# Kernel tuning notes

Measured on AMD Instinct MI355X. Metric: run time of the kernel, lower is better.

## Reference

```python
import jax, jax.numpy as jnp
import numpy as np

NUM_FREQUENCIES = 128
NUM_TIMES = 128
SIGMA = 0.1
BATCH = 32
LENGTH = 8192


def setup_inputs() -> dict:
    key = jax.random.key(0)
    signal = jax.random.normal(key, (BATCH, LENGTH), dtype=jnp.float32)
    return {"signal": signal}


def reference(signal) -> jnp.ndarray:
    # signal: [B, L]
    B, L = signal.shape
    # Matches torch.linspace(...).long(): linspace then truncate toward zero.
    time_centers = jnp.linspace(0.0, L - 1, NUM_TIMES).astype(jnp.int32).astype(jnp.float32)  # [T]
    freq_vals = jnp.linspace(0.0, L // 2, NUM_FREQUENCIES).astype(jnp.int32).astype(jnp.float32)  # [F]
    t = jnp.arange(L, dtype=jnp.float32)  # [L]
    sigma_w = SIGMA * L
    # Gaussian windows, one per time center: [T, L]
    window = jnp.exp(-0.5 * ((t[None, :] - time_centers[:, None]) / sigma_w) ** 2)
    # Real part of exp(-2j*pi*f*l/L) modulation: [F, L]
    two_pi = jnp.float32(2.0 * np.pi)
    cos_mod = jnp.cos(two_pi * freq_vals[:, None] * t[None, :] / L)
    # Original loop stores a complex dot product into a real tensor -> real part only:
    # result[b, f, t] = sum_l signal[b,l] * window[t,l] * cos(2*pi*f*l/L)
    windowed = jnp.einsum('bl,tl->btl', signal, window)  # [B, T, L]
    result = jnp.einsum('btl,fl->bft', windowed, cos_mod)  # [B, F, T]
    return result
```

## Files before the change

kernel.cpp:

```cpp
#include <hip/hip_runtime.h>
#include <hip/hip_bf16.h>
#include <math.h>


#define L_ 8192
#define B_ 32
#define SPLITK 16
#define KW 512
#define NSTEP 16

typedef _Float16 half8 __attribute__((ext_vector_type(8)));
typedef __fp16 fp16x2 __attribute__((ext_vector_type(2)));
typedef float float4v __attribute__((ext_vector_type(4)));

#define H_ 0.001220703125f
#define CSTEP_ 7.66990393942594528198e-4f


__global__ __launch_bounds__(256, 2) void gabor_gemm_kernel(
    const float* __restrict__ signal, float* __restrict__ partial) {
  const int bx = blockIdx.x;
  const int kc = bx & 15;
  const int bgrp = (bx >> 4) & 7;
  const int th = (bx >> 7) & 1;
  const int fh = (bx >> 8) & 1;
  const int tid = threadIdx.x;
  const int lane = tid & 63;
  const int wv = tid >> 6;
  const int frow = lane & 15;
  const int quad = lane >> 4;

  __shared__ _Float16 Sg[4][KW];

  {
    const int idx = tid * 8;
    const int bi = idx >> 9;
    const int off = idx & 511;
    const float* sp = signal + (size_t)(bgrp * 4 + bi) * L_ + kc * KW + off;
    float4v s0 = *(const float4v*)sp;
    float4v s1 = *(const float4v*)(sp + 4);
    union { fp16x2 h2[4]; half8 h8; } sh;
    sh.h2[0] = __builtin_amdgcn_cvt_pkrtz(s0[0], s0[1]);
    sh.h2[1] = __builtin_amdgcn_cvt_pkrtz(s0[2], s0[3]);
    sh.h2[2] = __builtin_amdgcn_cvt_pkrtz(s1[0], s1[1]);
    sh.h2[3] = __builtin_amdgcn_cvt_pkrtz(s1[2], s1[3]);
    *(half8*)&Sg[bi][off] = sh.h8;
  }
  __syncthreads();

  const int t0 = th * 64 + (wv & 1) * 32;
  const int f0 = fh * 64 + (wv >> 1) * 32;
  const int l0 = kc * KW + quad * 8;

  float w[2][8], Rw[2][8];
  const float Q32 = __expf(-0.00152587890625f);
#pragma unroll
  for (int fr = 0; fr < 2; ++fr) {
    const float tc = truncf((float)(t0 + fr * 16 + frow) * (8191.0f / 127.0f));
#pragma unroll
    for (int j = 0; j < 8; ++j) {
      const float x = ((float)(l0 + j) - tc) * H_;
      w[fr][j] = __expf(-0.5f * x * x);
      Rw[fr][j] = __expf(__builtin_fmaf(-0.0390625f, x, -7.62939453125e-4f));
    }
  }
  float c[2][8], cp[2][8], K32[2];
#pragma unroll
  for (int fr = 0; fr < 2; ++fr) {
    const int fv = (int)((float)(f0 + fr * 16 + frow) * (4096.0f / 127.0f));
    K32[fr] = 2.0f * __cosf((float)((fv * 32) & (L_ - 1)) * CSTEP_);
#pragma unroll
    for (int j = 0; j < 8; ++j) {
      c[fr][j] = __cosf((float)((fv * (l0 + j)) & (L_ - 1)) * CSTEP_);
      cp[fr][j] = __cosf((float)((fv * (l0 + j + 8160)) & (L_ - 1)) * CSTEP_);
    }
  }

  float4v acc[2][2][4];
#pragma unroll
  for (int i = 0; i < 2; ++i)
#pragma unroll
    for (int j = 0; j < 2; ++j)
#pragma unroll
      for (int bi = 0; bi < 4; ++bi) acc[i][j][bi] = (float4v)(0.0f);

#pragma unroll
  for (int s = 0; s < NSTEP; ++s) {
    union { fp16x2 h2[4]; half8 h8; } ha[2], hc[2];
#pragma unroll
    for (int fr = 0; fr < 2; ++fr)
#pragma unroll
      for (int p = 0; p < 4; ++p) {
        ha[fr].h2[p] = __builtin_amdgcn_cvt_pkrtz(w[fr][2 * p], w[fr][2 * p + 1]);
        hc[fr].h2[p] = __builtin_amdgcn_cvt_pkrtz(c[fr][2 * p], c[fr][2 * p + 1]);
      }
    half8 sgv[4];
#pragma unroll
    for (int bi = 0; bi < 4; ++bi)
      sgv[bi] = *(const half8*)&Sg[bi][s * 32 + quad * 8];
#pragma unroll
    for (int fr2 = 0; fr2 < 2; ++fr2)
#pragma unroll
      for (int bi = 0; bi < 4; ++bi) {
        const half8 hbf = hc[fr2].h8 * sgv[bi];
        acc[0][fr2][bi] = __builtin_amdgcn_mfma_f32_16x16x32_f16(
            ha[0].h8, hbf, acc[0][fr2][bi], 0, 0, 0);
        acc[1][fr2][bi] = __builtin_amdgcn_mfma_f32_16x16x32_f16(
            ha[1].h8, hbf, acc[1][fr2][bi], 0, 0, 0);
      }
    if (s + 1 < NSTEP) {
#pragma unroll
      for (int fr = 0; fr < 2; ++fr)
#pragma unroll
        for (int j = 0; j < 8; ++j) {
          w[fr][j] *= Rw[fr][j];
          Rw[fr][j] *= Q32;
          const float cn = __builtin_fmaf(K32[fr], c[fr][j], -cp[fr][j]);
          cp[fr][j] = c[fr][j];
          c[fr][j] = cn;
        }
    }
  }

#pragma unroll
  for (int bi = 0; bi < 4; ++bi) {
    float* pbase = partial + ((size_t)(kc * B_ + bgrp * 4 + bi) << 14);
#pragma unroll
    for (int fr2 = 0; fr2 < 2; ++fr2) {
      const int f = f0 + fr2 * 16 + frow;
#pragma unroll
      for (int fr1 = 0; fr1 < 2; ++fr1) {
        const int t = t0 + fr1 * 16 + quad * 4;
        *(float4v*)(pbase + f * 128 + t) = acc[fr1][fr2][bi];
      }
    }
  }
}

__global__ __launch_bounds__(256) void gabor_reduce_kernel(
    const float* __restrict__ partial, float* __restrict__ out) {
  const size_t gi = ((size_t)blockIdx.x * 256 + threadIdx.x) * 4;
  float4v s = (float4v)(0.0f);
#pragma unroll
  for (int kc = 0; kc < SPLITK; ++kc)
    s += *(const float4v*)(partial + (size_t)kc * 524288 + gi);
  *(float4v*)(out + gi) = s;
}

extern "C" void kernel_launch(void* const* d_in, const int* in_sizes, int n_in,
                              void* d_out, int out_size, void* d_ws, size_t ws_size,
                              hipStream_t stream) {
  const float* signal = (const float*)d_in[0];
  float* out = (float*)d_out;
  float* partial = (float*)d_ws;
  gabor_gemm_kernel<<<dim3(512), dim3(256), 0, stream>>>(signal, partial);
  gabor_reduce_kernel<<<dim3(512), dim3(256), 0, stream>>>(partial, out);
}
```

Baseline: 81.17 us.

## Fuse split-K reduction into one kernel with per-batch blocks and in-block wave reduction

Replaces the two-kernel split-K scheme, which wrote 16 partial sums to global memory and then reduced them in a second kernel, with a single kernel. Each block now handles one batch row over the full length. The four waves split K, and their accumulators are summed through shared memory before a direct store to the output. The inner loop switches to packed float2 recurrences with an unroll-1 loop of 32 double steps, which cuts register pressure. In exchange, each block runs a much longer recurrence chain, which risks fp16/fp32 drift, and each wave now does one batch instead of four, so there is less reuse of the A operand per MFMA.

```diff
diff --git a/kernel.cpp b/kernel.cpp
--- a/kernel.cpp
+++ b/kernel.cpp
@@ -5,146 +5,153 @@
 
 #define L_ 8192
 #define B_ 32
-#define SPLITK 16
-#define KW 512
-#define NSTEP 16
 
 typedef _Float16 half8 __attribute__((ext_vector_type(8)));
 typedef __fp16 fp16x2 __attribute__((ext_vector_type(2)));
+typedef float float2v __attribute__((ext_vector_type(2)));
 typedef float float4v __attribute__((ext_vector_type(4)));
 
 #define H_ 0.001220703125f
 #define CSTEP_ 7.66990393942594528198e-4f
 
-
-__global__ __launch_bounds__(256, 2) void gabor_gemm_kernel(
-    const float* __restrict__ signal, float* __restrict__ partial) {
+__global__ __launch_bounds__(256, 2) void gabor_kernel(
+    const float* __restrict__ signal, float* __restrict__ out) {
   const int bx = blockIdx.x;
-  const int kc = bx & 15;
-  const int bgrp = (bx >> 4) & 7;
-  const int th = (bx >> 7) & 1;
-  const int fh = (bx >> 8) & 1;
+  const int b = bx & 31;
+  const int th = (bx >> 5) & 3;
+  const int fh = (bx >> 7) & 3;
   const int tid = threadIdx.x;
   const int lane = tid & 63;
   const int wv = tid >> 6;
   const int frow = lane & 15;
   const int quad = lane >> 4;
 
-  __shared__ _Float16 Sg[4][KW];
+  __shared__ _Float16 Sg[L_];
+  __shared__ float4v Acc[4][64][4];
 
   {
-    const int idx = tid * 8;
-    const int bi = idx >> 9;
-    const int off = idx & 511;
-    const float* sp = signal + (size_t)(bgrp * 4 + bi) * L_ + kc * KW + off;
-    float4v s0 = *(const float4v*)sp;
-    float4v s1 = *(const float4v*)(sp + 4);
-    union { fp16x2 h2[4]; half8 h8; } sh;
-    sh.h2[0] = __builtin_amdgcn_cvt_pkrtz(s0[0], s0[1]);
-    sh.h2[1] = __builtin_amdgcn_cvt_pkrtz(s0[2], s0[3]);
-    sh.h2[2] = __builtin_amdgcn_cvt_pkrtz(s1[0], s1[1]);
-    sh.h2[3] = __builtin_amdgcn_cvt_pkrtz(s1[2], s1[3]);
-    *(half8*)&Sg[bi][off] = sh.h8;
+    const float* srow = signal + (size_t)b * L_;
+#pragma unroll
+    for (int i = 0; i < 4; ++i) {
+      const int off = i * 2048 + tid * 8;
+      float4v s0 = *(const float4v*)(srow + off);
+      float4v s1 = *(const float4v*)(srow + off + 4);
+      union { fp16x2 h2[4]; half8 h8; } sh;
+      sh.h2[0] = __builtin_amdgcn_cvt_pkrtz(s0[0], s0[1]);
+      sh.h2[1] = __builtin_amdgcn_cvt_pkrtz(s0[2], s0[3]);
+      sh.h2[2] = __builtin_amdgcn_cvt_pkrtz(s1[0], s1[1]);
+      sh.h2[3] = __builtin_amdgcn_cvt_pkrtz(s1[2], s1[3]);
+      *(half8*)&Sg[off] = sh.h8;
+    }
   }
   __syncthreads();
 
-  const int t0 = th * 64 + (wv & 1) * 32;
-  const int f0 = fh * 64 + (wv >> 1) * 32;
-  const int l0 = kc * KW + quad * 8;
+  const int t0 = th * 32;
+  const int f0 = fh * 32;
+  const int k0 = wv * 2048 + quad * 8;
 
-  float w[2][8], Rw[2][8];
-  const float Q32 = __expf(-0.00152587890625f);
+  float2v w2[2][4], Rw2[2][4];
+  float2v cE2[2][4], cO2[2][4];
+  float2v K32v[2];
+  const float2v Q32v = {0.99847528338432312012f, 0.99847528338432312012f};
 #pragma unroll
   for (int fr = 0; fr < 2; ++fr) {
     const float tc = truncf((float)(t0 + fr * 16 + frow) * (8191.0f / 127.0f));
+    const int fv = (int)((float)(f0 + fr * 16 + frow) * (4096.0f / 127.0f));
+    const float K32 = 2.0f * __cosf((float)((fv * 32) & (L_ - 1)) * CSTEP_);
+    K32v[fr] = (float2v){K32, K32};
 #pragma unroll
-    for (int j = 0; j < 8; ++j) {
-      const float x = ((float)(l0 + j) - tc) * H_;
-      w[fr][j] = __expf(-0.5f * x * x);
-      Rw[fr][j] = __expf(__builtin_fmaf(-0.0390625f, x, -7.62939453125e-4f));
-    }
-  }
-  float c[2][8], cp[2][8], K32[2];
+    for (int q = 0; q < 4; ++q) {
 #pragma unroll
-  for (int fr = 0; fr < 2; ++fr) {
-    const int fv = (int)((float)(f0 + fr * 16 + frow) * (4096.0f / 127.0f));
-    K32[fr] = 2.0f * __cosf((float)((fv * 32) & (L_ - 1)) * CSTEP_);
-#pragma unroll
-    for (int j = 0; j < 8; ++j) {
-      c[fr][j] = __cosf((float)((fv * (l0 + j)) & (L_ - 1)) * CSTEP_);
-      cp[fr][j] = __cosf((float)((fv * (l0 + j + 8160)) & (L_ - 1)) * CSTEP_);
+      for (int h = 0; h < 2; ++h) {
+        const int j = 2 * q + h;
+        const float x = ((float)(k0 + j) - tc) * H_;
+        w2[fr][q][h] = __expf(-0.5f * x * x);
+        Rw2[fr][q][h] =
+            __expf(__builtin_fmaf(-0.0390625f, x, -7.62939453125e-4f));
+        cE2[fr][q][h] = __cosf((float)((fv * (k0 + j)) & (L_ - 1)) * CSTEP_);
+        cO2[fr][q][h] =
+            __cosf((float)((fv * (k0 + j + 8160)) & (L_ - 1)) * CSTEP_);
+      }
     }
   }
 
-  float4v acc[2][2][4];
+  float4v acc[2][2];
 #pragma unroll
   for (int i = 0; i < 2; ++i)
 #pragma unroll
-    for (int j = 0; j < 2; ++j)
-#pragma unroll
-      for (int bi = 0; bi < 4; ++bi) acc[i][j][bi] = (float4v)(0.0f);
+    for (int j = 0; j < 2; ++j) acc[i][j] = (float4v)(0.0f);
 
-#pragma unroll
-  for (int s = 0; s < NSTEP; ++s) {
-    union { fp16x2 h2[4]; half8 h8; } ha[2], hc[2];
-#pragma unroll
-    for (int fr = 0; fr < 2; ++fr)
-#pragma unroll
-      for (int p = 0; p < 4; ++p) {
-        ha[fr].h2[p] = __builtin_amdgcn_cvt_pkrtz(w[fr][2 * p], w[fr][2 * p + 1]);
-        hc[fr].h2[p] = __builtin_amdgcn_cvt_pkrtz(c[fr][2 * p], c[fr][2 * p + 1]);
-      }
-    half8 sgv[4];
-#pragma unroll
-    for (int bi = 0; bi < 4; ++bi)
-      sgv[bi] = *(const half8*)&Sg[bi][s * 32 + quad * 8];
-#pragma unroll
-    for (int fr2 = 0; fr2 < 2; ++fr2)
-#pragma unroll
-      for (int bi = 0; bi < 4; ++bi) {
-        const half8 hbf = hc[fr2].h8 * sgv[bi];
-        acc[0][fr2][bi] = __builtin_amdgcn_mfma_f32_16x16x32_f16(
-            ha[0].h8, hbf, acc[0][fr2][bi], 0, 0, 0);
-        acc[1][fr2][bi] = __builtin_amdgcn_mfma_f32_16x16x32_f16(
-            ha[1].h8, hbf, acc[1][fr2][bi], 0, 0, 0);
-      }
-    if (s + 1 < NSTEP) {
+  union H8 { fp16x2 h2[4]; half8 h8; };
+
+#pragma unroll 1
+  for (int p = 0; p < 32; ++p) {
+    {
+      H8 ha[2], hc[2];
 #pragma unroll
       for (int fr = 0; fr < 2; ++fr)
 #pragma unroll
-        for (int j = 0; j < 8; ++j) {
-          w[fr][j] *= Rw[fr][j];
-          Rw[fr][j] *= Q32;
-          const float cn = __builtin_fmaf(K32[fr], c[fr][j], -cp[fr][j]);
-          cp[fr][j] = c[fr][j];
-          c[fr][j] = cn;
+        for (int q = 0; q < 4; ++q) {
+          ha[fr].h2[q] = __builtin_amdgcn_cvt_pkrtz(w2[fr][q][0], w2[fr][q][1]);
+          hc[fr].h2[q] = __builtin_amdgcn_cvt_pkrtz(cE2[fr][q][0], cE2[fr][q][1]);
+        }
+      const half8 sgv = *(const half8*)&Sg[k0 + (2 * p) * 32];
+#pragma unroll
+      for (int fr2 = 0; fr2 < 2; ++fr2) {
+        const half8 hbf = hc[fr2].h8 * sgv;
+        acc[0][fr2] = __builtin_amdgcn_mfma_f32_16x16x32_f16(ha[0].h8, hbf,
+                                                             acc[0][fr2], 0, 0, 0);
+        acc[1][fr2] = __builtin_amdgcn_mfma_f32_16x16x32_f16(ha[1].h8, hbf,
+                                                             acc[1][fr2], 0, 0, 0);
+      }
+#pragma unroll
+      for (int fr = 0; fr < 2; ++fr)
+#pragma unroll
+        for (int q = 0; q < 4; ++q) {
+          w2[fr][q] *= Rw2[fr][q];
+          Rw2[fr][q] *= Q32v;
+          cO2[fr][q] = __builtin_elementwise_fma(K32v[fr], cE2[fr][q], -cO2[fr][q]);
+        }
+    }
+    {
+      H8 ha[2], hc[2];
+#pragma unroll
+      for (int fr = 0; fr < 2; ++fr)
+#pragma unroll
+        for (int q = 0; q < 4; ++q) {
+          ha[fr].h2[q] = __builtin_amdgcn_cvt_pkrtz(w2[fr][q][0], w2[fr][q][1]);
+          hc[fr].h2[q] = __builtin_amdgcn_cvt_pkrtz(cO2[fr][q][0], cO2[fr][q][1]);
+        }
+      const half8 sgv = *(const half8*)&Sg[k0 + (2 * p + 1) * 32];
+#pragma unroll
+      for (int fr2 = 0; fr2 < 2; ++fr2) {
+        const half8 hbf = hc[fr2].h8 * sgv;
+        acc[0][fr2] = __builtin_amdgcn_mfma_f32_16x16x32_f16(ha[0].h8, hbf,
+                                                             acc[0][fr2], 0, 0, 0);
+        acc[1][fr2] = __builtin_amdgcn_mfma_f32_16x16x32_f16(ha[1].h8, hbf,
+                                                             acc[1][fr2], 0, 0, 0);
+      }
+#pragma unroll
+      for (int fr = 0; fr < 2; ++fr)
+#pragma unroll
+        for (int q = 0; q < 4; ++q) {
+          w2[fr][q] *= Rw2[fr][q];
+          Rw2[fr][q] *= Q32v;
+          cE2[fr][q] = __builtin_elementwise_fma(K32v[fr], cO2[fr][q], -cE2[fr][q]);
         }
     }
   }
 
 #pragma unroll
-  for (int bi = 0; bi < 4; ++bi) {
-    float* pbase = partial + ((size_t)(kc * B_ + bgrp * 4 + bi) << 14);
-#pragma unroll
-    for (int fr2 = 0; fr2 < 2; ++fr2) {
-      const int f = f0 + fr2 * 16 + frow;
-#pragma unroll
-      for (int fr1 = 0; fr1 < 2; ++fr1) {
-        const int t = t0 + fr1 * 16 + quad * 4;
-        *(float4v*)(pbase + f * 128 + t) = acc[fr1][fr2][bi];
-      }
-    }
-  }
-}
-
-__global__ __launch_bounds__(256) void gabor_reduce_kernel(
-    const float* __restrict__ partial, float* __restrict__ out) {
-  const size_t gi = ((size_t)blockIdx.x * 256 + threadIdx.x) * 4;
-  float4v s = (float4v)(0.0f);
-#pragma unroll
-  for (int kc = 0; kc < SPLITK; ++kc)
-    s += *(const float4v*)(partial + (size_t)kc * 524288 + gi);
-  *(float4v*)(out + gi) = s;
+  for (int i4 = 0; i4 < 4; ++i4)
+    Acc[wv][lane][i4] = acc[i4 >> 1][i4 & 1];
+  __syncthreads();
+  float4v sum = Acc[0][lane][wv] + Acc[1][lane][wv] +
+                Acc[2][lane][wv] + Acc[3][lane][wv];
+  const int fr1 = wv >> 1, fr2 = wv & 1;
+  const int f = f0 + fr2 * 16 + frow;
+  const int t = t0 + fr1 * 16 + quad * 4;
+  *(float4v*)(out + ((size_t)(b * 128 + f)) * 128 + t) = sum;
 }
 
 extern "C" void kernel_launch(void* const* d_in, const int* in_sizes, int n_in,
@@ -152,7 +159,5 @@
                               hipStream_t stream) {
   const float* signal = (const float*)d_in[0];
   float* out = (float*)d_out;
-  float* partial = (float*)d_ws;
-  gabor_gemm_kernel<<<dim3(512), dim3(256), 0, stream>>>(signal, partial);
-  gabor_reduce_kernel<<<dim3(512), dim3(256), 0, stream>>>(partial, out);
+  gabor_kernel<<<dim3(512), dim3(256), 0, stream>>>(signal, out);
 }
```

Result: faster. 70.92 us (-12.6%).
